# Kernel tuning notes

Measured on AMD Instinct MI355X. Metric: run time of the kernel, lower is better.

Reference implementation:

```python
import jax, jax.numpy as jnp
import numpy as np

N = 50000      # nodes
E = 800000     # edges (avg degree 16)
F_IN = 128     # input features
H, C = 4, 16   # heads, per-head out channels -> conv out = 64
D = 128        # target_dim (proj output)
NEG_SLOPE = 0.2
LN_EPS = 1e-5


def setup_inputs() -> dict:
    key = jax.random.key(0)
    ks = jax.random.split(key, 8)
    s_in = 1.0 / np.sqrt(F_IN)
    s_hc = 1.0 / np.sqrt(H * C)
    return {
        "x": jax.random.normal(ks[0], (N, F_IN), jnp.float32),
        "edge_index": jax.random.randint(ks[1], (2, E), 0, N, jnp.int64),
        "W": jax.random.normal(ks[2], (F_IN, H * C), jnp.float32) * s_in,
        "att_src": jax.random.normal(ks[3], (H, C), jnp.float32) * s_hc,
        "att_dst": jax.random.normal(ks[4], (H, C), jnp.float32) * s_hc,
        "bias": jnp.zeros((H * C,), jnp.float32),
        "proj_w": jax.random.normal(ks[5], (D, H * C), jnp.float32) * s_hc,
        "proj_b": jnp.zeros((D,), jnp.float32),
        "gamma": jnp.ones((D,), jnp.float32),
        "beta": jnp.zeros((D,), jnp.float32),
    }


def reference(x, edge_index, W, att_src, att_dst, bias, proj_w, proj_b, gamma, beta):
    src, dst = edge_index[0], edge_index[1]
    # GATConv: per-head linear transform  [N, H, C]
    xp = (x @ W).reshape(N, H, C)
    a_src = jnp.einsum("nhc,hc->nh", xp, att_src)  # [N, H]
    a_dst = jnp.einsum("nhc,hc->nh", xp, att_dst)  # [N, H]
    # raw attention logits per edge, per head  [E, H]
    e = jax.nn.leaky_relu(a_src[src] + a_dst[dst], NEG_SLOPE)
    # segment softmax over incoming edges of each destination node
    m = jax.ops.segment_max(e, dst, num_segments=N)          # [N, H]
    ex = jnp.exp(e - m[dst])                                 # [E, H]
    denom = jax.ops.segment_sum(ex, dst, num_segments=N)     # [N, H]
    alpha = ex / (denom[dst] + 1e-16)                        # [E, H]
    # weighted message aggregation  [N, H, C]
    out = jax.ops.segment_sum(alpha[:, :, None] * xp[src], dst, num_segments=N)
    out = out.reshape(N, H * C) + bias                       # concat heads
    # projection to target_dim
    out = out @ proj_w.T + proj_b                            # [N, D]
    # LayerNorm over feature dim
    mu = out.mean(axis=-1, keepdims=True)
    var = out.var(axis=-1, keepdims=True)
    out = (out - mu) * jax.lax.rsqrt(var + LN_EPS) * gamma + beta
    # activation (relu); dropout=0.0 -> identity
    return jax.nn.relu(out)
```

## Files before the change

kernel.cpp:

```cpp
#include <hip/hip_runtime.h>
#include <hip/hip_bf16.h>


#define LEAKY(x) ((x) > 0.f ? (x) : 0.2f * (x))
#define CHUNK 2048
#define NBUK_PAD 256

typedef __attribute__((ext_vector_type(8))) short bf16x8;
typedef __attribute__((ext_vector_type(8))) unsigned short u16x8;
typedef __attribute__((ext_vector_type(4))) float f32x4;

static __device__ __forceinline__ unsigned short f2bf_rne(float f) {
    unsigned u = __float_as_uint(f);
    return (unsigned short)((u + 0x7FFFu + ((u >> 16) & 1u)) >> 16);
}
static __device__ __forceinline__ float bf2f(unsigned short h) {
    return __uint_as_float(((unsigned)h) << 16);
}

__global__ __launch_bounds__(256) void k_prep_part1(
    const float* __restrict__ W, const float* __restrict__ bias,
    const float* __restrict__ proj_w, const float* __restrict__ proj_b,
    unsigned short* __restrict__ Whf, unsigned short* __restrict__ Wlf,
    unsigned short* __restrict__ Phf, unsigned short* __restrict__ Plf,
    float* __restrict__ pb2,
    const int* __restrict__ dst, int* __restrict__ cnt, int E, int nchunk)
{
    int bid = blockIdx.x, t = threadIdx.x;
    if (bid < nchunk) {
        __shared__ int hist[NBUK_PAD];
        hist[t] = 0;
        __syncthreads();
        int e0 = bid * CHUNK;
#pragma unroll
        for (int i = 0; i < CHUNK / 256; i++) {
            int e = e0 + i * 256 + t;
            if (e < E) atomicAdd(&hist[dst[e] >> 8], 1);
        }
        __syncthreads();
        cnt[bid * NBUK_PAD + t] = hist[t];
        return;
    }
    int idx = (bid - nchunk) * 256 + t;
    if (idx < 8192) {
        int j = idx & 7, lane = (idx >> 3) & 63, ts = idx >> 9;
        int tt = ts >> 2, s = ts & 3;
        int k = s * 32 + ((lane >> 4) << 3) + j;
        int n = tt * 16 + (lane & 15);
        float w = W[k * 64 + n];
        unsigned short wh = f2bf_rne(w);
        Whf[idx] = wh;
        Wlf[idx] = f2bf_rne(w - bf2f(wh));
    } else if (idx < 16384) {
        int i2 = idx - 8192;
        int j = i2 & 7, lane = (i2 >> 3) & 63, ts = i2 >> 9;
        int tt = ts >> 1, s = ts & 1;
        int k = s * 32 + ((lane >> 4) << 3) + j;
        int d = tt * 16 + (lane & 15);
        float w = proj_w[d * 64 + k];
        unsigned short wh = f2bf_rne(w);
        Phf[i2] = wh;
        Plf[i2] = f2bf_rne(w - bf2f(wh));
    } else if (idx < 16384 + 128) {
        int d = idx - 16384;
        float s = proj_b[d];
        for (int j = 0; j < 64; j++) s += bias[j] * proj_w[d * 64 + j];
        pb2[d] = s;
    }
}

__global__ __launch_bounds__(256) void k_scanB1(int* __restrict__ cnt, int* __restrict__ bt,
                                                int* __restrict__ row_ptr,
                                                int nchunk, int n_nodes, int E)
{
    __shared__ int sh[256];
    int t = threadIdx.x, b = blockIdx.x;
    int v0 = (t < nchunk) ? cnt[t * NBUK_PAD + b] : 0;
    int v1 = (t + 256 < nchunk) ? cnt[(t + 256) * NBUK_PAD + b] : 0;
    sh[t] = v0; __syncthreads();
    for (int off = 1; off < 256; off <<= 1) {
        int u = (t >= off) ? sh[t - off] : 0;
        __syncthreads();
        sh[t] += u;
        __syncthreads();
    }
    int incl0 = sh[t], tot0 = sh[255];
    __syncthreads();
    sh[t] = v1; __syncthreads();
    for (int off = 1; off < 256; off <<= 1) {
        int u = (t >= off) ? sh[t - off] : 0;
        __syncthreads();
        sh[t] += u;
        __syncthreads();
    }
    int incl1 = sh[t] + tot0;
    if (t < nchunk) cnt[t * NBUK_PAD + b] = incl0 - v0;
    if (t + 256 < nchunk) cnt[(t + 256) * NBUK_PAD + b] = incl1 - v1;
    if (t == 255) bt[b] = incl1;
    if (b == 0 && t == 0) row_ptr[n_nodes] = E;
}

__global__ __launch_bounds__(256) void k_part2_xw(
    const int* __restrict__ src, const int* __restrict__ dst,
    const int* __restrict__ cnt, const int* __restrict__ bt,
    unsigned* __restrict__ part, int E,
    const float* __restrict__ x,
    const unsigned short* __restrict__ Whf, const unsigned short* __restrict__ Wlf,
    const float* __restrict__ att_src, const float* __restrict__ att_dst,
    unsigned short* __restrict__ xp, float* __restrict__ a_src, float* __restrict__ a_dst,
    int n_nodes, int P, int nbXw)
{
    __shared__ float xs[64][132];
    __shared__ int bases[NBUK_PAD];
    __shared__ int sh[256];
    int bid = blockIdx.x, t = threadIdx.x;
    if (bid % P == P - 1) {
        int blk = bid / P;
        int v = bt[t];
        sh[t] = v; __syncthreads();
        for (int off = 1; off < 256; off <<= 1) {
            int u = (t >= off) ? sh[t - off] : 0;
            __syncthreads();
            sh[t] += u;
            __syncthreads();
        }
        bases[t] = cnt[blk * NBUK_PAD + t] + (sh[t] - v);
        __syncthreads();
        int e0 = blk * CHUNK;
#pragma unroll
        for (int i = 0; i < CHUNK / 256; i++) {
            int e = e0 + i * 256 + t;
            if (e < E) {
                int d = dst[e];
                int s = src[e];
                int pos = atomicAdd(&bases[d >> 8], 1);
                part[pos] = ((unsigned)s << 8) | (unsigned)(d & 255);
            }
        }
        return;
    }
    int xb = bid - bid / P;
    if (xb >= nbXw) return;
    int xbase = xb * 64;
    for (int i = t; i < 64 * 32; i += 256) {
        int r = i >> 5, c = (i & 31) << 2;
        int gr = xbase + r; if (gr >= n_nodes) gr = n_nodes - 1;
        *(float4*)&xs[r][c] = *(const float4*)(x + (size_t)gr * 128 + c);
    }
    __syncthreads();
    int w = t >> 6, lane = t & 63;
    int mbase = xbase + w * 16;
    int mrow = lane & 15, kg = lane >> 4;
    int lrow = w * 16 + mrow;

    bf16x8 ah[4], al[4];
#pragma unroll
    for (int s = 0; s < 4; s++) {
        float4 v0 = *(const float4*)&xs[lrow][s * 32 + kg * 8];
        float4 v1 = *(const float4*)&xs[lrow][s * 32 + kg * 8 + 4];
        float f[8] = {v0.x, v0.y, v0.z, v0.w, v1.x, v1.y, v1.z, v1.w};
#pragma unroll
        for (int j = 0; j < 8; j++) {
            unsigned short h = f2bf_rne(f[j]);
            ah[s][j] = (short)h;
            al[s][j] = (short)f2bf_rne(f[j] - bf2f(h));
        }
    }

    f32x4 acc[4];
#pragma unroll
    for (int tt = 0; tt < 4; tt++) acc[tt] = (f32x4){0.f, 0.f, 0.f, 0.f};
#pragma unroll
    for (int tt = 0; tt < 4; tt++) {
#pragma unroll
        for (int s = 0; s < 4; s++) {
            size_t fi = (size_t)(((tt * 4 + s) * 64 + lane) * 8);
            bf16x8 bh = *(const bf16x8*)(Whf + fi);
            bf16x8 bl = *(const bf16x8*)(Wlf + fi);
            acc[tt] = __builtin_amdgcn_mfma_f32_16x16x32_bf16(ah[s], bh, acc[tt], 0, 0, 0);
            acc[tt] = __builtin_amdgcn_mfma_f32_16x16x32_bf16(ah[s], bl, acc[tt], 0, 0, 0);
            acc[tt] = __builtin_amdgcn_mfma_f32_16x16x32_bf16(al[s], bh, acc[tt], 0, 0, 0);
        }
    }

#pragma unroll
    for (int tt = 0; tt < 4; tt++) {
        float asv = att_src[tt * 16 + mrow];
        float adv = att_dst[tt * 16 + mrow];
#pragma unroll
        for (int r = 0; r < 4; r++) {
            float v = acc[tt][r];
            int n2 = mbase + kg * 4 + r;
            bool ok = (n2 < n_nodes);
            if (ok) xp[(size_t)n2 * 64 + tt * 16 + mrow] = f2bf_rne(v);
            float ts = v * asv;
            float td = v * adv;
#pragma unroll
            for (int off = 8; off; off >>= 1) {
                ts += __shfl_xor(ts, off);
                td += __shfl_xor(td, off);
            }
            if (mrow == 0 && ok) {
                a_src[n2 * 4 + tt] = ts;
                a_dst[n2 * 4 + tt] = td;
            }
        }
    }
}

__global__ __launch_bounds__(256) void k_csr(const unsigned* __restrict__ part, const int* __restrict__ bt,
                                             int* __restrict__ row_ptr, int* __restrict__ colsrc,
                                             int n_nodes)
{
    __shared__ int hist[256], off[256], sh[256];
    int t = threadIdx.x, b = blockIdx.x;
    int v = bt[t];
    sh[t] = v; __syncthreads();
    for (int o = 1; o < 256; o <<= 1) {
        int u = (t >= o) ? sh[t - o] : 0;
        __syncthreads();
        sh[t] += u;
        __syncthreads();
    }
    int e0 = (b > 0) ? sh[b - 1] : 0;
    int e1 = sh[b];
    __syncthreads();
    int m = e1 - e0;
    hist[t] = 0;
    __syncthreads();
    for (int i = t; i < m; i += 256)
        atomicAdd(&hist[part[e0 + i] & 255u], 1);
    __syncthreads();
    int hv = hist[t];
    sh[t] = hv; __syncthreads();
    for (int o = 1; o < 256; o <<= 1) {
        int u = (t >= o) ? sh[t - o] : 0;
        __syncthreads();
        sh[t] += u;
        __syncthreads();
    }
    int excl = sh[t] - hv;
    off[t] = excl;
    int node = b * 256 + t;
    if (node < n_nodes) row_ptr[node] = e0 + excl;
    __syncthreads();
    for (int i = t; i < m; i += 256) {
        unsigned u = part[e0 + i];
        int pos = atomicAdd(&off[u & 255u], 1);
        colsrc[e0 + pos] = (int)(u >> 8);
    }
}

__global__ __launch_bounds__(256, 6) void k_agg_proj(
    const unsigned short* __restrict__ xp, const float* __restrict__ a_src, const float* __restrict__ a_dst,
    const int* __restrict__ row_ptr, const int* __restrict__ colsrc,
    const unsigned short* __restrict__ Phf, const unsigned short* __restrict__ Plf,
    const float* __restrict__ pb2, const float* __restrict__ gamma, const float* __restrict__ beta,
    float* __restrict__ out, int n_nodes)
{
    __shared__ int   sstage[4][64];
    __shared__ float alpha_s[4][64][4];
    __shared__ unsigned short rowbuf[16][72];
    __shared__ float pS[4][16], pQ[4][16];
    __shared__ float pb_s[128], g_s[128], b_s[128];
    int t = threadIdx.x, w = t >> 6, lane = t & 63;
    if (t < 128) { pb_s[t] = pb2[t]; g_s[t] = gamma[t]; b_s[t] = beta[t]; }
    int cgrp = lane & 7;
    int eoct = lane >> 3;
    int h = cgrp >> 1;
    int nb16 = blockIdx.x * 16;

    for (int i = 0; i < 4; i++) {
        int n = nb16 + w * 4 + i;
        int nl = w * 4 + i;
        float acc[8] = {0.f,0.f,0.f,0.f,0.f,0.f,0.f,0.f};
        float den = 0.f;
        if (n < n_nodes) {
            int rp0 = row_ptr[n], rp1 = row_ptr[n + 1];
            float4 ad4 = *(const float4*)&a_dst[(size_t)n * 4];
            for (int base = rp0; base < rp1; base += 64) {
                int cnt = rp1 - base; if (cnt > 64) cnt = 64;
                int s = 0;
                float4 p = make_float4(0.f, 0.f, 0.f, 0.f);
                if (lane < cnt) {
                    s = colsrc[base + lane];
                    float4 as4 = *(const float4*)&a_src[(size_t)s * 4];
                    p.x = __expf(LEAKY(as4.x + ad4.x));
                    p.y = __expf(LEAKY(as4.y + ad4.y));
                    p.z = __expf(LEAKY(as4.z + ad4.z));
                    p.w = __expf(LEAKY(as4.w + ad4.w));
                }
                sstage[w][lane] = s;
                *(float4*)&alpha_s[w][lane][0] = p;
                int iters = (cnt + 7) >> 3;
                for (int it = 0; it < iters; ++it) {
                    int j = (it << 3) + eoct;
                    int sj = sstage[w][j];
                    float aj = alpha_s[w][j][h];
                    u16x8 v = *(const u16x8*)(xp + (size_t)((unsigned)sj * 64u + (cgrp << 3)));
                    den += aj;
#pragma unroll
                    for (int q = 0; q < 8; q++) acc[q] += aj * bf2f(v[q]);
                }
            }
#pragma unroll
            for (int q = 0; q < 8; q++) {
                acc[q] += __shfl_xor(acc[q], 8);
                acc[q] += __shfl_xor(acc[q], 16);
                acc[q] += __shfl_xor(acc[q], 32);
            }
            den += __shfl_xor(den, 8);
            den += __shfl_xor(den, 16);
            den += __shfl_xor(den, 32);
        }
        if (eoct == 0) {
            float inv = 1.f / (den + 1e-16f);
            u16x8 o;
#pragma unroll
            for (int q = 0; q < 8; q++) o[q] = f2bf_rne(acc[q] * inv);
            *(u16x8*)&rowbuf[nl][cgrp << 3] = o;
        }
    }
    __syncthreads();

    int mrow = lane & 15, kg = lane >> 4;
    bf16x8 ah[2];
#pragma unroll
    for (int s = 0; s < 2; s++) {
        ah[s] = *(const bf16x8*)&rowbuf[mrow][s * 32 + kg * 8];
    }
    f32x4 acc2[2];
#pragma unroll
    for (int ttl = 0; ttl < 2; ttl++) acc2[ttl] = (f32x4){0.f, 0.f, 0.f, 0.f};
#pragma unroll
    for (int ttl = 0; ttl < 2; ttl++) {
        int tt = w * 2 + ttl;
#pragma unroll
        for (int s = 0; s < 2; s++) {
            size_t fi = (size_t)(((tt * 2 + s) * 64 + lane) * 8);
            bf16x8 bh = *(const bf16x8*)(Phf + fi);
            bf16x8 bl = *(const bf16x8*)(Plf + fi);
            acc2[ttl] = __builtin_amdgcn_mfma_f32_16x16x32_bf16(ah[s], bh, acc2[ttl], 0, 0, 0);
            acc2[ttl] = __builtin_amdgcn_mfma_f32_16x16x32_bf16(ah[s], bl, acc2[ttl], 0, 0, 0);
        }
    }
    float vv[2][4];
#pragma unroll
    for (int r = 0; r < 4; r++) {
        float S = 0.f, Q = 0.f;
#pragma unroll
        for (int ttl = 0; ttl < 2; ttl++) {
            int tt = w * 2 + ttl;
            float v = acc2[ttl][r] + pb_s[tt * 16 + mrow];
            vv[ttl][r] = v;
            S += v;
            Q += v * v;
        }
#pragma unroll
        for (int off = 8; off; off >>= 1) {
            S += __shfl_xor(S, off);
            Q += __shfl_xor(Q, off);
        }
        if (mrow == 0) { pS[w][kg * 4 + r] = S; pQ[w][kg * 4 + r] = Q; }
    }
    __syncthreads();
#pragma unroll
    for (int r = 0; r < 4; r++) {
        int nl = kg * 4 + r;
        int nr = nb16 + nl;
        float S = pS[0][nl] + pS[1][nl] + pS[2][nl] + pS[3][nl];
        float Q = pQ[0][nl] + pQ[1][nl] + pQ[2][nl] + pQ[3][nl];
        float mu  = S * (1.f / 128.f);
        float var = Q * (1.f / 128.f) - mu * mu;
        float inv = rsqrtf(var + 1e-5f);
        if (nr < n_nodes) {
#pragma unroll
            for (int ttl = 0; ttl < 2; ttl++) {
                int d = (w * 2 + ttl) * 16 + mrow;
                float o = fmaxf((vv[ttl][r] - mu) * inv * g_s[d] + b_s[d], 0.f);
                out[(size_t)nr * 128 + d] = o;
            }
        }
    }
}

extern "C" void kernel_launch(void* const* d_in, const int* in_sizes, int n_in,
                              void* d_out, int out_size, void* d_ws, size_t ws_size,
                              hipStream_t stream)
{
    const float* x       = (const float*)d_in[0];
    const int*   ei      = (const int*)  d_in[1];
    const float* W       = (const float*)d_in[2];
    const float* att_src = (const float*)d_in[3];
    const float* att_dst = (const float*)d_in[4];
    const float* bias    = (const float*)d_in[5];
    const float* proj_w  = (const float*)d_in[6];
    const float* proj_b  = (const float*)d_in[7];
    const float* gamma   = (const float*)d_in[8];
    const float* beta    = (const float*)d_in[9];

    int N = in_sizes[0] / 128;
    int E = in_sizes[1] / 2;
    const int* srcIdx = ei;
    const int* dstIdx = ei + E;

    int nchunk = (E + CHUNK - 1) / CHUNK;
    int NBUK   = (N + 255) / 256;
    int nbXw   = (N + 63) / 64;
    int nbPrep = (16512 + 255) / 256;

    char* ws = (char*)d_ws;
    unsigned short* xp = (unsigned short*)ws; ws += (size_t)N * 64 * 2;
    float* a_src   = (float*)ws; ws += (size_t)N * 4 * 4;
    float* a_dst   = (float*)ws; ws += (size_t)N * 4 * 4;
    int*   row_ptr = (int*)ws;   ws += (size_t)(N + 1) * 4;
    int*   cnt     = (int*)ws;   ws += (size_t)nchunk * NBUK_PAD * 4;
    unsigned* part = (unsigned*)ws; ws += (size_t)E * 4;
    int*   colsrc  = (int*)ws;   ws += (size_t)E * 4;
    int*   bt      = (int*)ws;   ws += 256 * 4;
    unsigned short* Whf = (unsigned short*)ws; ws += 8192 * 2;
    unsigned short* Wlf = (unsigned short*)ws; ws += 8192 * 2;
    unsigned short* Phf = (unsigned short*)ws; ws += 8192 * 2;
    unsigned short* Plf = (unsigned short*)ws; ws += 8192 * 2;
    float* pb2 = (float*)ws; ws += 128 * 4;

    int P = (nbXw + nchunk - 1) / nchunk + 1;
    int totalFused = nchunk * P;

    k_prep_part1<<<nchunk + nbPrep, 256, 0, stream>>>(W, bias, proj_w, proj_b,
                                                      Whf, Wlf, Phf, Plf, pb2,
                                                      dstIdx, cnt, E, nchunk);
    k_scanB1<<<256, 256, 0, stream>>>(cnt, bt, row_ptr, nchunk, N, E);
    k_part2_xw<<<totalFused, 256, 0, stream>>>(srcIdx, dstIdx, cnt, bt, part, E,
                                               x, Whf, Wlf, att_src, att_dst,
                                               xp, a_src, a_dst, N, P, nbXw);
    k_csr<<<NBUK, 256, 0, stream>>>(part, bt, row_ptr, colsrc, N);
    k_agg_proj<<<(N + 15) / 16, 256, 0, stream>>>(xp, a_src, a_dst, row_ptr, colsrc,
                                                  Phf, Plf, pb2, gamma, beta,
                                                  (float*)d_out, N);
}
```

Baseline: 83.52 us.

## Software-pipeline per-node edge loads in aggregation and enlarge partition chunks

The aggregation kernel now batch-loads row_ptr and a_dst for a wave's four nodes once. It also double-buffers the LDS staging, so the colsrc and a_src loads for the next node are issued while the current node's feature gather runs. The aim is to hide the dependent colsrc→a_src→xp load latency chain. Separately, CHUNK grows from 2048 to 8192 with partial unrolling, which cuts the number of histogram and partition blocks and the size of the count table. The tradeoffs are fewer blocks, and so less parallelism and more LDS atomic contention per block, plus more registers and LDS in the aggregation kernel.

```diff
diff --git a/kernel.cpp b/kernel.cpp
--- a/kernel.cpp
+++ b/kernel.cpp
@@ -3,7 +3,7 @@
 
 
 #define LEAKY(x) ((x) > 0.f ? (x) : 0.2f * (x))
-#define CHUNK 2048
+#define CHUNK 8192
 #define NBUK_PAD 256
 
 typedef __attribute__((ext_vector_type(8))) short bf16x8;
@@ -32,7 +32,7 @@
         hist[t] = 0;
         __syncthreads();
         int e0 = bid * CHUNK;
-#pragma unroll
+#pragma unroll 4
         for (int i = 0; i < CHUNK / 256; i++) {
             int e = e0 + i * 256 + t;
             if (e < E) atomicAdd(&hist[dst[e] >> 8], 1);
@@ -127,7 +127,7 @@
         bases[t] = cnt[blk * NBUK_PAD + t] + (sh[t] - v);
         __syncthreads();
         int e0 = blk * CHUNK;
-#pragma unroll
+#pragma unroll 4
         for (int i = 0; i < CHUNK / 256; i++) {
             int e = e0 + i * 256 + t;
             if (e < E) {
@@ -256,10 +256,10 @@
     const int* __restrict__ row_ptr, const int* __restrict__ colsrc,
     const unsigned short* __restrict__ Phf, const unsigned short* __restrict__ Plf,
     const float* __restrict__ pb2, const float* __restrict__ gamma, const float* __restrict__ beta,
-    float* __restrict__ out, int n_nodes)
+    float* __restrict__ out, int n_nodes, int E)
 {
-    __shared__ int   sstage[4][64];
-    __shared__ float alpha_s[4][64][4];
+    __shared__ int   sstage[4][2][64];
+    __shared__ float alpha_s[4][2][64][4];
     __shared__ unsigned short rowbuf[16][72];
     __shared__ float pS[4][16], pQ[4][16];
     __shared__ float pb_s[128], g_s[128], b_s[128];
@@ -269,58 +269,131 @@
     int eoct = lane >> 3;
     int h = cgrp >> 1;
     int nb16 = blockIdx.x * 16;
-
-    for (int i = 0; i < 4; i++) {
-        int n = nb16 + w * 4 + i;
-        int nl = w * 4 + i;
+    int nbw = nb16 + w * 4;
+
+    int rpv = 0;
+    {
+        int idx = nbw + lane;
+        if (idx > n_nodes) idx = n_nodes;
+        if (lane < 5) rpv = row_ptr[idx];
+    }
+    float adv = 0.f;
+    {
+        long idx = (long)nbw * 4 + lane;
+        long mx = (long)n_nodes * 4 - 1;
+        if (idx > mx) idx = mx;
+        if (lane < 16) adv = a_dst[idx];
+    }
+
+    auto ldcol = [&](int i) -> int {
+        int rp0 = __shfl(rpv, i), rp1 = __shfl(rpv, i + 1);
+        int cb = rp1 - rp0; if (cb > 64) cb = 64;
+        int a = (lane < cb) ? rp0 + lane : rp0;
+        if (a >= E) a = 0;
+        return colsrc[a];
+    };
+    auto lda = [&](int s) -> float4 {
+        return *(const float4*)&a_src[(size_t)(unsigned)s * 4];
+    };
+    auto finish = [&](int i, int bi, int s, float4 as4) {
+        int rp0 = __shfl(rpv, i), rp1 = __shfl(rpv, i + 1);
+        int cb = rp1 - rp0; if (cb > 64) cb = 64;
+        float adx = __shfl(adv, (i << 2) + 0);
+        float ady = __shfl(adv, (i << 2) + 1);
+        float adz = __shfl(adv, (i << 2) + 2);
+        float adw = __shfl(adv, (i << 2) + 3);
+        float4 p = make_float4(0.f, 0.f, 0.f, 0.f);
+        if (lane < cb) {
+            p.x = __expf(LEAKY(as4.x + adx));
+            p.y = __expf(LEAKY(as4.y + ady));
+            p.z = __expf(LEAKY(as4.z + adz));
+            p.w = __expf(LEAKY(as4.w + adw));
+        }
+        sstage[w][bi][lane] = s;
+        *(float4*)&alpha_s[w][bi][lane][0] = p;
+    };
+    auto gather = [&](int i, int bi) {
+        int rp0 = __shfl(rpv, i), rp1 = __shfl(rpv, i + 1);
+        int deg = rp1 - rp0;
         float acc[8] = {0.f,0.f,0.f,0.f,0.f,0.f,0.f,0.f};
         float den = 0.f;
-        if (n < n_nodes) {
-            int rp0 = row_ptr[n], rp1 = row_ptr[n + 1];
-            float4 ad4 = *(const float4*)&a_dst[(size_t)n * 4];
-            for (int base = rp0; base < rp1; base += 64) {
-                int cnt = rp1 - base; if (cnt > 64) cnt = 64;
-                int s = 0;
-                float4 p = make_float4(0.f, 0.f, 0.f, 0.f);
-                if (lane < cnt) {
-                    s = colsrc[base + lane];
-                    float4 as4 = *(const float4*)&a_src[(size_t)s * 4];
-                    p.x = __expf(LEAKY(as4.x + ad4.x));
-                    p.y = __expf(LEAKY(as4.y + ad4.y));
-                    p.z = __expf(LEAKY(as4.z + ad4.z));
-                    p.w = __expf(LEAKY(as4.w + ad4.w));
-                }
-                sstage[w][lane] = s;
-                *(float4*)&alpha_s[w][lane][0] = p;
-                int iters = (cnt + 7) >> 3;
-                for (int it = 0; it < iters; ++it) {
-                    int j = (it << 3) + eoct;
-                    int sj = sstage[w][j];
-                    float aj = alpha_s[w][j][h];
-                    u16x8 v = *(const u16x8*)(xp + (size_t)((unsigned)sj * 64u + (cgrp << 3)));
-                    den += aj;
-#pragma unroll
-                    for (int q = 0; q < 8; q++) acc[q] += aj * bf2f(v[q]);
-                }
+        int cb = deg > 64 ? 64 : deg;
+        int iters = (cb + 7) >> 3;
+        for (int it = 0; it < iters; ++it) {
+            int j = (it << 3) + eoct;
+            int sj = sstage[w][bi][j];
+            float aj = alpha_s[w][bi][j][h];
+            u16x8 v = *(const u16x8*)(xp + (size_t)((unsigned)sj * 64u + (cgrp << 3)));
+            den += aj;
+#pragma unroll
+            for (int q = 0; q < 8; q++) acc[q] += aj * bf2f(v[q]);
+        }
+        for (int b0 = 64; b0 < deg; b0 += 64) {
+            int cbx = deg - b0; if (cbx > 64) cbx = 64;
+            int a = (lane < cbx) ? rp0 + b0 + lane : rp0;
+            if (a >= E) a = 0;
+            int s = colsrc[a];
+            float4 as4 = lda(s);
+            finish_tail:;
+            float adx = __shfl(adv, (i << 2) + 0);
+            float ady = __shfl(adv, (i << 2) + 1);
+            float adz = __shfl(adv, (i << 2) + 2);
+            float adw = __shfl(adv, (i << 2) + 3);
+            float4 p = make_float4(0.f, 0.f, 0.f, 0.f);
+            if (lane < cbx) {
+                p.x = __expf(LEAKY(as4.x + adx));
+                p.y = __expf(LEAKY(as4.y + ady));
+                p.z = __expf(LEAKY(as4.z + adz));
+                p.w = __expf(LEAKY(as4.w + adw));
             }
-#pragma unroll
-            for (int q = 0; q < 8; q++) {
-                acc[q] += __shfl_xor(acc[q], 8);
-                acc[q] += __shfl_xor(acc[q], 16);
-                acc[q] += __shfl_xor(acc[q], 32);
+            sstage[w][bi][lane] = s;
+            *(float4*)&alpha_s[w][bi][lane][0] = p;
+            int it2 = (cbx + 7) >> 3;
+            for (int it = 0; it < it2; ++it) {
+                int j = (it << 3) + eoct;
+                int sj = sstage[w][bi][j];
+                float aj = alpha_s[w][bi][j][h];
+                u16x8 v = *(const u16x8*)(xp + (size_t)((unsigned)sj * 64u + (cgrp << 3)));
+                den += aj;
+#pragma unroll
+                for (int q = 0; q < 8; q++) acc[q] += aj * bf2f(v[q]);
             }
-            den += __shfl_xor(den, 8);
-            den += __shfl_xor(den, 16);
-            den += __shfl_xor(den, 32);
-        }
+        }
+#pragma unroll
+        for (int q = 0; q < 8; q++) {
+            acc[q] += __shfl_xor(acc[q], 8);
+            acc[q] += __shfl_xor(acc[q], 16);
+            acc[q] += __shfl_xor(acc[q], 32);
+        }
+        den += __shfl_xor(den, 8);
+        den += __shfl_xor(den, 16);
+        den += __shfl_xor(den, 32);
         if (eoct == 0) {
             float inv = 1.f / (den + 1e-16f);
             u16x8 o;
 #pragma unroll
             for (int q = 0; q < 8; q++) o[q] = f2bf_rne(acc[q] * inv);
-            *(u16x8*)&rowbuf[nl][cgrp << 3] = o;
-        }
-    }
+            *(u16x8*)&rowbuf[w * 4 + i][cgrp << 3] = o;
+        }
+    };
+
+    int   s0 = ldcol(0);
+    float4 a0 = lda(s0);
+    finish(0, 0, s0, a0);
+    int   s1 = ldcol(1);
+    float4 a1 = lda(s1);
+    int   s2 = ldcol(2);
+    gather(0, 0);
+    finish(1, 1, s1, a1);
+    float4 a2 = lda(s2);
+    int   s3 = ldcol(3);
+    gather(1, 1);
+    finish(2, 0, s2, a2);
+    float4 a3 = lda(s3);
+    gather(2, 0);
+    finish(3, 1, s3, a3);
+    gather(3, 1);
+
     __syncthreads();
 
     int mrow = lane & 15, kg = lane >> 4;
@@ -437,5 +510,5 @@
     k_csr<<<NBUK, 256, 0, stream>>>(part, bt, row_ptr, colsrc, N);
     k_agg_proj<<<(N + 15) / 16, 256, 0, stream>>>(xp, a_src, a_dst, row_ptr, colsrc,
                                                   Phf, Plf, pb2, gamma, beta,
-                                                  (float*)d_out, N);
-}
+                                                  (float*)d_out, N, E);
+}
```

Result: slower. 91.63 us (+9.7%).
